# Optimization experiments

Hardware: AMD Instinct MI355X
Metric: run time of the kernel (lower is better)

The kernel has to match this reference:

```python
import jax, jax.numpy as jnp
import numpy as np
import math

DIM = 1024
NUM_HEAD = 16
HEAD_DIM = DIM // NUM_HEAD


def setup_inputs() -> dict:
    key = jax.random.key(0)
    ks = jax.random.split(key, 4)
    B, L = 4, 2048
    x = jax.random.normal(ks[0], (B, L, DIM), dtype=jnp.float32)
    # Linear weights stored as [in, out]; scaled like torch default init (~1/sqrt(in)).
    w_qkv = jax.random.normal(ks[1], (DIM, 3 * DIM), dtype=jnp.float32) / math.sqrt(DIM)
    b_qkv = jnp.zeros((3 * DIM,), dtype=jnp.float32)
    w_out = jax.random.normal(ks[2], (DIM, DIM), dtype=jnp.float32) / math.sqrt(DIM)
    b_out = jnp.zeros((DIM,), dtype=jnp.float32)
    return {"x": x, "w_qkv": w_qkv, "b_qkv": b_qkv, "w_out": w_out, "b_out": b_out}


def _attn(x, w_qkv, b_qkv, w_out, b_out):
    B, L, D = x.shape
    qkv = x @ w_qkv + b_qkv                      # [B, L, 3D]
    q, k, v = jnp.split(qkv, 3, axis=-1)         # each [B, L, D]
    def heads(t):
        return t.reshape(B, L, NUM_HEAD, HEAD_DIM).transpose(0, 2, 1, 3)  # [B,H,L,d]
    q, k, v = heads(q), heads(k), heads(v)
    scale = 1.0 / math.sqrt(HEAD_DIM)
    w = jnp.einsum('bhqd,bhkd->bhqk', q, k) * scale   # [B,H,L,L]
    causal = jnp.tril(jnp.ones((L, L), dtype=bool))
    w = jnp.where(causal, w, -jnp.inf)
    w = jax.nn.softmax(w, axis=-1)               # dropout_p = 0 -> identity
    out = jnp.einsum('bhqk,bhkd->bhqd', w, v)    # [B,H,L,d]
    out = out.transpose(0, 2, 1, 3).reshape(B, L, D)
    return out @ w_out + b_out


def reference(x, w_qkv, b_qkv, w_out, b_out):
    return _attn(x, w_qkv, b_qkv, w_out, b_out)
```

## Files before the change

### kernel.cpp

```cpp
#include <hip/hip_runtime.h>

typedef __bf16 bf16;
typedef __attribute__((ext_vector_type(8))) __bf16 bf16x8;
typedef __attribute__((ext_vector_type(4))) __bf16 bf16x4;
typedef __attribute__((ext_vector_type(4))) float f32x4;

#define MFMA16(a, b, c) __builtin_amdgcn_mfma_f32_16x16x32_bf16((a), (b), (c), 0, 0, 0)


static __device__ __forceinline__ bf16x8 cvt_f4x2(const float4 a, const float4 b) {
  bf16x8 r;
  r[0] = (bf16)a.x; r[1] = (bf16)a.y; r[2] = (bf16)a.z; r[3] = (bf16)a.w;
  r[4] = (bf16)b.x; r[5] = (bf16)b.y; r[6] = (bf16)b.z; r[7] = (bf16)b.w;
  return r;
}

static __device__ __forceinline__ void gll16(const bf16* g, bf16* l) {
  __builtin_amdgcn_global_load_lds(
      (const __attribute__((address_space(1))) void*)g,
      (__attribute__((address_space(3))) void*)l, 16, 0, 0);
}

__global__ __launch_bounds__(256) void conv_x_kernel(const float* __restrict__ X,
                                                     bf16* __restrict__ Xb) {
  const size_t i = ((size_t)blockIdx.x * 256 + threadIdx.x) * 16;
  const float4* s = (const float4*)&X[i];
  *(bf16x8*)&Xb[i] = cvt_f4x2(s[0], s[1]);
  *(bf16x8*)&Xb[i + 8] = cvt_f4x2(s[2], s[3]);
}

__global__ __launch_bounds__(256) void conv_w_kernel(
    const float* __restrict__ W, bf16* __restrict__ Wt, int Nw) {
  __shared__ bf16 sT[64][72];
  const int tid = threadIdx.x;
  const int n0 = blockIdx.x * 64, k0 = blockIdx.y * 64;
  const int kr = tid >> 4;
  const int c4 = (tid & 15) * 4;
#pragma unroll
  for (int i = 0; i < 4; ++i) {
    const int k = kr + i * 16;
    const float4 w4 = *(const float4*)&W[(size_t)(k0 + k) * Nw + n0 + c4];
    sT[c4 + 0][k] = (bf16)w4.x;
    sT[c4 + 1][k] = (bf16)w4.y;
    sT[c4 + 2][k] = (bf16)w4.z;
    sT[c4 + 3][k] = (bf16)w4.w;
  }
  __syncthreads();
  const int r = tid >> 2;
  const int c8 = (tid & 3) * 16;
  *(bf16x8*)&Wt[(size_t)(n0 + r) * 1024 + k0 + c8] = *(const bf16x8*)&sT[r][c8];
  *(bf16x8*)&Wt[(size_t)(n0 + r) * 1024 + k0 + c8 + 8] =
      *(const bf16x8*)&sT[r][c8 + 8];
}

static __device__ __forceinline__ void qkv_epilogue(
    f32x4 acc[4][4], const float* bias, bf16* Qb, bf16* Kb, bf16* Vt, int m0,
    int n0, int wr, int wc, int lg, int lr) {
  if (n0 < 2048) {
    bf16* dst = (n0 < 1024) ? Qb : Kb;
#pragma unroll
    for (int m = 0; m < 4; ++m) {
#pragma unroll
      for (int n = 0; n < 4; ++n) {
        const int colg = n0 + wc * 64 + n * 16 + lr;
        const int col = colg & 1023;
        const int h = col >> 6, d = col & 63;
        const float bv = bias[colg];
#pragma unroll
        for (int i = 0; i < 4; ++i) {
          const int row = m0 + wr * 64 + m * 16 + lg * 4 + i;
          const int bb = row >> 11, ll = row & 2047;
          dst[((size_t)((bb * 16 + h) * 2048 + ll)) * 64 + d] =
              (bf16)(acc[m][n][i] + bv);
        }
      }
    }
  } else {
#pragma unroll
    for (int m = 0; m < 4; ++m) {
#pragma unroll
      for (int n = 0; n < 4; ++n) {
        const int colg = n0 + wc * 64 + n * 16 + lr;
        const int col = colg & 1023;
        const int h = col >> 6, d = col & 63;
        const float bv = bias[colg];
        const int row0 = m0 + wr * 64 + m * 16 + lg * 4;
        const int bb = row0 >> 11, ll0 = row0 & 2047;
        bf16x4 pk;
#pragma unroll
        for (int i = 0; i < 4; ++i) pk[i] = (bf16)(acc[m][n][i] + bv);
        *(bf16x4*)&Vt[((size_t)((bb * 16 + h) * 64 + d)) * 2048 + ll0] = pk;
      }
    }
  }
}

__global__ __launch_bounds__(256) void gemm_qkv_bf16_kernel(
    const bf16* __restrict__ Xb, const bf16* __restrict__ Wt,
    const float* __restrict__ bias, bf16* __restrict__ Qb,
    bf16* __restrict__ Kb, bf16* __restrict__ Vt) {
  constexpr int K = 1024;
  __shared__ __align__(16) bf16 sA[128 * 64];
  __shared__ __align__(16) bf16 sB[128 * 64];
  const int tid = threadIdx.x;
  const int m0 = blockIdx.y * 128, n0 = blockIdx.x * 128;
  const int wid = tid >> 6, lane = tid & 63;
  const int wr = wid >> 1, wc = wid & 1;
  const int lg = lane >> 4, lr = lane & 15;

  const f32x4 fz = {0.f, 0.f, 0.f, 0.f};
  f32x4 acc[4][4];
#pragma unroll
  for (int m = 0; m < 4; ++m)
#pragma unroll
    for (int n = 0; n < 4; ++n) acc[m][n] = fz;

  for (int k0 = 0; k0 < K; k0 += 64) {
#pragma unroll
    for (int s = 0; s < 4; ++s) {
      const int off = s * 2048 + tid * 8;
      const int row = off >> 6, col = off & 63;
      gll16(&Xb[(size_t)(m0 + row) * K + k0 + col], &sA[off]);
      gll16(&Wt[(size_t)(n0 + row) * K + k0 + col], &sB[off]);
    }
    __syncthreads();

    bf16x8 af[2][4], bfv[2][4];
#pragma unroll
    for (int ks = 0; ks < 2; ++ks) {
#pragma unroll
      for (int m = 0; m < 4; ++m)
        af[ks][m] = *(const bf16x8*)&sA[(wr * 64 + m * 16 + lr) * 64 + ks * 32 + 8 * lg];
#pragma unroll
      for (int n = 0; n < 4; ++n)
        bfv[ks][n] = *(const bf16x8*)&sB[(wc * 64 + n * 16 + lr) * 64 + ks * 32 + 8 * lg];
    }
#pragma unroll
    for (int ks = 0; ks < 2; ++ks)
#pragma unroll
      for (int m = 0; m < 4; ++m)
#pragma unroll
        for (int n = 0; n < 4; ++n)
          acc[m][n] = MFMA16(af[ks][m], bfv[ks][n], acc[m][n]);
    __syncthreads();
  }
  qkv_epilogue(acc, bias, Qb, Kb, Vt, m0, n0, wr, wc, lg, lr);
}

__global__ __launch_bounds__(256) void gemm_qkv_kernel(
    const float* __restrict__ X, const bf16* __restrict__ Wt,
    const float* __restrict__ bias, bf16* __restrict__ Qb,
    bf16* __restrict__ Kb, bf16* __restrict__ Vt) {
  constexpr int K = 1024;
  __shared__ __align__(16) bf16 sA[128 * 64];
  __shared__ __align__(16) bf16 sB[128 * 64];
  const int tid = threadIdx.x;
  const int m0 = blockIdx.y * 128, n0 = blockIdx.x * 128;
  const int wid = tid >> 6, lane = tid & 63;
  const int wr = wid >> 1, wc = wid & 1;
  const int lg = lane >> 4, lr = lane & 15;

  const f32x4 fz = {0.f, 0.f, 0.f, 0.f};
  f32x4 acc[4][4];
#pragma unroll
  for (int m = 0; m < 4; ++m)
#pragma unroll
    for (int n = 0; n < 4; ++n) acc[m][n] = fz;

  for (int k0 = 0; k0 < K; k0 += 64) {
#pragma unroll
    for (int s = 0; s < 4; ++s) {
      const int off = s * 2048 + tid * 8;
      const int row = off >> 6, col = off & 63;
      gll16(&Wt[(size_t)(n0 + row) * K + k0 + col], &sB[off]);
    }
#pragma unroll
    for (int p = 0; p < 4; ++p) {
      const int g = tid + p * 256;
      const int row = g >> 3, c8 = (g & 7) * 8;
      const float4* src = (const float4*)&X[(size_t)(m0 + row) * K + k0 + c8];
      const float4 u = src[0], w = src[1];
      *(bf16x8*)&sA[row * 64 + c8] = cvt_f4x2(u, w);
    }
    __syncthreads();

    bf16x8 af[2][4], bfv[2][4];
#pragma unroll
    for (int ks = 0; ks < 2; ++ks) {
#pragma unroll
      for (int m = 0; m < 4; ++m)
        af[ks][m] = *(const bf16x8*)&sA[(wr * 64 + m * 16 + lr) * 64 + ks * 32 + 8 * lg];
#pragma unroll
      for (int n = 0; n < 4; ++n)
        bfv[ks][n] = *(const bf16x8*)&sB[(wc * 64 + n * 16 + lr) * 64 + ks * 32 + 8 * lg];
    }
#pragma unroll
    for (int ks = 0; ks < 2; ++ks)
#pragma unroll
      for (int m = 0; m < 4; ++m)
#pragma unroll
        for (int n = 0; n < 4; ++n)
          acc[m][n] = MFMA16(af[ks][m], bfv[ks][n], acc[m][n]);
    __syncthreads();
  }
  qkv_epilogue(acc, bias, Qb, Kb, Vt, m0, n0, wr, wc, lg, lr);
}

#define ATTN_FULL 0
#define ATTN_MASK 1
#define ATTN_SKIP 2

__global__ __launch_bounds__(256, 3) void attn_kernel(
    const bf16* __restrict__ Qb, const bf16* __restrict__ Kb,
    const bf16* __restrict__ Vt, bf16* __restrict__ O) {
  __shared__ __align__(16) bf16 sK[2][64 * 64];
  __shared__ __align__(16) bf16 sV[2][64 * 64];
  __shared__ __align__(16) bf16 sP[4][16 * 72];
  const int tid = threadIdx.x;
  const int qb = 15 - (int)(blockIdx.x >> 6);
  const int bh = blockIdx.x & 63;
  const int q0 = qb * 128;
  const int nt = 2 * qb + 2;
  const int wid = tid >> 6, lane = tid & 63;
  const int lg = lane >> 4, lr = lane & 15;
  const bf16* Kbh = Kb + (size_t)bh * (2048 * 64);
  const bf16* Vth = Vt + (size_t)bh * (64 * 2048);
  bf16* sPw = &sP[wid][0];
  const int swz = (lr & 7) << 3;

  const int qrow0 = q0 + wid * 16 + lr;
  const int qrow1 = qrow0 + 64;
  bf16x8 qf[2][2];
#pragma unroll
  for (int h = 0; h < 2; ++h) {
    const bf16* qp =
        Qb + (size_t)bh * (2048 * 64) + (size_t)(qrow0 + 64 * h) * 64 + 8 * lg;
    qf[h][0] = *(const bf16x8*)qp;
    qf[h][1] = *(const bf16x8*)(qp + 32);
#pragma unroll
    for (int j = 0; j < 8; ++j) {
      qf[h][0][j] = (bf16)((float)qf[h][0][j] * 0.125f);
      qf[h][1][j] = (bf16)((float)qf[h][1][j] * 0.125f);
    }
  }

  const int pe = tid * 8;
  const int srow0 = pe >> 6;
  const int scol0 = (pe & 63) ^ ((srow0 & 7) << 3);
  const int srow1 = srow0 + 32;
  const int scol1 = (pe & 63) ^ ((srow1 & 7) << 3);

  const f32x4 fz = {0.f, 0.f, 0.f, 0.f};
  f32x4 o[2][4];
#pragma unroll
  for (int h = 0; h < 2; ++h)
#pragma unroll
    for (int n = 0; n < 4; ++n) o[h][n] = fz;
  float m_[2] = {-1e30f, -1e30f}, ssum[2] = {0.f, 0.f};

#define STAGE(buf, kv0_)                                                      \
  {                                                                           \
    const int kv0s = (kv0_);                                                  \
    gll16(&Kbh[(size_t)(kv0s + srow0) * 64 + scol0], &sK[buf][pe]);           \
    gll16(&Kbh[(size_t)(kv0s + srow1) * 64 + scol1], &sK[buf][2048 + pe]);    \
    gll16(&Vth[(size_t)srow0 * 2048 + kv0s + scol0], &sV[buf][pe]);           \
    gll16(&Vth[(size_t)srow1 * 2048 + kv0s + scol1], &sV[buf][2048 + pe]);    \
  }

  STAGE(0, 0);

  for (int t = 0; t < nt; ++t) {
    const int buf = t & 1;
    const int kv0 = t * 64;
    const int mode0 = (t < nt - 2) ? ATTN_FULL : (t == nt - 2 ? ATTN_MASK : ATTN_SKIP);
    const int mode1 = (t < nt - 1) ? ATTN_FULL : ATTN_MASK;

    __builtin_amdgcn_s_barrier();
    if (t + 1 < nt) {
      STAGE(buf ^ 1, kv0 + 64);
      asm volatile("s_waitcnt vmcnt(4)" ::: "memory");
    } else {
      asm volatile("s_waitcnt vmcnt(0)" ::: "memory");
    }
    __builtin_amdgcn_s_barrier();

    const bf16* sKb = sK[buf];
    const bf16* sVb = sV[buf];

    f32x4 s0[4], s1[4];
    __builtin_amdgcn_s_setprio(1);
#pragma unroll
    for (int sub = 0; sub < 4; ++sub) {
      const int e = ((sub * 16 + lr) * 64 + 8 * lg) ^ swz;
      const bf16x8 kf0 = *(const bf16x8*)&sKb[e];
      const bf16x8 kf1 = *(const bf16x8*)&sKb[e ^ 32];
      if (mode0 != ATTN_SKIP) {
        f32x4 sc = MFMA16(kf0, qf[0][0], fz);
        s0[sub] = MFMA16(kf1, qf[0][1], sc);
      }
      f32x4 sc = MFMA16(kf0, qf[1][0], fz);
      s1[sub] = MFMA16(kf1, qf[1][1], sc);
    }
    __builtin_amdgcn_s_setprio(0);

    bf16x8 vf[4][2];
#pragma unroll
    for (int n = 0; n < 4; ++n)
#pragma unroll
      for (int c2 = 0; c2 < 2; ++c2)
        vf[n][c2] = *(const bf16x8*)&sVb[(((n * 16 + lr) * 64 + c2 * 32 + 8 * lg)) ^ swz];

#pragma unroll
    for (int h = 0; h < 2; ++h) {
      const int mode = h ? mode1 : mode0;
      if (mode == ATTN_SKIP) continue;
      const int qrow = h ? qrow1 : qrow0;
      f32x4* sh = h ? s1 : s0;

      float sv[16];
      float rm = -3e30f;
#pragma unroll
      for (int sub = 0; sub < 4; ++sub)
#pragma unroll
        for (int i = 0; i < 4; ++i) {
          float v = sh[sub][i];
          if (mode == ATTN_MASK) {
            const int kvg = kv0 + sub * 16 + lg * 4 + i;
            v = (kvg > qrow) ? -3e30f : v;
          }
          sv[sub * 4 + i] = v;
          rm = fmaxf(rm, v);
        }
      rm = fmaxf(rm, __shfl_xor(rm, 16));
      rm = fmaxf(rm, __shfl_xor(rm, 32));
      if (!__all(rm <= m_[h] + 8.f)) {
        const float mn = fmaxf(m_[h], rm);
        const float corr = __expf(m_[h] - mn);
        ssum[h] *= corr;
        m_[h] = mn;
        float cr[4];
#pragma unroll
        for (int i = 0; i < 4; ++i) cr[i] = __shfl(corr, 4 * lg + i);
#pragma unroll
        for (int n = 0; n < 4; ++n)
#pragma unroll
          for (int i = 0; i < 4; ++i) o[h][n][i] *= cr[i];
      }
      float rs = 0.f;
#pragma unroll
      for (int sub = 0; sub < 4; ++sub) {
        bf16x4 pk;
#pragma unroll
        for (int i = 0; i < 4; ++i) {
          const float p = __expf(sv[sub * 4 + i] - m_[h]);
          rs += p;
          pk[i] = (bf16)p;
        }
        *(bf16x4*)&sPw[lr * 72 + 16 * sub + 4 * lg] = pk;
      }
      rs += __shfl_xor(rs, 16);
      rs += __shfl_xor(rs, 32);
      ssum[h] += rs;
      __builtin_amdgcn_s_setprio(1);
#pragma unroll
      for (int c2 = 0; c2 < 2; ++c2) {
        const bf16x8 pf = *(const bf16x8*)&sPw[lr * 72 + 32 * c2 + 8 * lg];
#pragma unroll
        for (int n = 0; n < 4; ++n) o[h][n] = MFMA16(pf, vf[n][c2], o[h][n]);
      }
      __builtin_amdgcn_s_setprio(0);
    }
  }
#undef STAGE

  const int b = bh >> 4, hh = bh & 15;
#pragma unroll
  for (int h = 0; h < 2; ++h) {
    const float rinv = 1.f / ssum[h];
    float rv[4];
#pragma unroll
    for (int i = 0; i < 4; ++i) rv[i] = __shfl(rinv, 4 * lg + i);
#pragma unroll
    for (int n = 0; n < 4; ++n)
#pragma unroll
      for (int i = 0; i < 4; ++i) {
        const int q = q0 + 64 * h + wid * 16 + 4 * lg + i;
        O[((size_t)(b * 2048 + q)) * 1024 + hh * 64 + n * 16 + lr] =
            (bf16)(o[h][n][i] * rv[i]);
      }
  }
}

__global__ __launch_bounds__(256) void gemm_out_kernel(
    const bf16* __restrict__ A, const bf16* __restrict__ Wt,
    const float* __restrict__ bias, float* __restrict__ Out) {
  constexpr int K = 1024, N = 1024;
  __shared__ __align__(16) bf16 sA[128 * 64];
  __shared__ __align__(16) bf16 sB[128 * 64];
  const int tid = threadIdx.x;
  const int m0 = blockIdx.y * 128, n0 = blockIdx.x * 128;
  const int wid = tid >> 6, lane = tid & 63;
  const int wr = wid >> 1, wc = wid & 1;
  const int lg = lane >> 4, lr = lane & 15;

  const f32x4 fz = {0.f, 0.f, 0.f, 0.f};
  f32x4 acc[4][4];
#pragma unroll
  for (int m = 0; m < 4; ++m)
#pragma unroll
    for (int n = 0; n < 4; ++n) acc[m][n] = fz;

  for (int k0 = 0; k0 < K; k0 += 64) {
#pragma unroll
    for (int s = 0; s < 4; ++s) {
      const int off = s * 2048 + tid * 8;
      const int row = off >> 6, col = off & 63;
      gll16(&A[(size_t)(m0 + row) * K + k0 + col], &sA[off]);
      gll16(&Wt[(size_t)(n0 + row) * K + k0 + col], &sB[off]);
    }
    __syncthreads();

    bf16x8 af[2][4], bfv[2][4];
#pragma unroll
    for (int ks = 0; ks < 2; ++ks) {
#pragma unroll
      for (int m = 0; m < 4; ++m)
        af[ks][m] = *(const bf16x8*)&sA[(wr * 64 + m * 16 + lr) * 64 + ks * 32 + 8 * lg];
#pragma unroll
      for (int n = 0; n < 4; ++n)
        bfv[ks][n] = *(const bf16x8*)&sB[(wc * 64 + n * 16 + lr) * 64 + ks * 32 + 8 * lg];
    }
#pragma unroll
    for (int ks = 0; ks < 2; ++ks)
#pragma unroll
      for (int m = 0; m < 4; ++m)
#pragma unroll
        for (int n = 0; n < 4; ++n)
          acc[m][n] = MFMA16(af[ks][m], bfv[ks][n], acc[m][n]);
    __syncthreads();
  }

#pragma unroll
  for (int m = 0; m < 4; ++m) {
#pragma unroll
    for (int n = 0; n < 4; ++n) {
      const int colg = n0 + wc * 64 + n * 16 + lr;
      const float bv = bias[colg];
#pragma unroll
      for (int i = 0; i < 4; ++i) {
        const int row = m0 + wr * 64 + m * 16 + lg * 4 + i;
        Out[(size_t)row * N + colg] = acc[m][n][i] + bv;
      }
    }
  }
}

extern "C" void kernel_launch(void* const* d_in, const int* in_sizes, int n_in,
                              void* d_out, int out_size, void* d_ws,
                              size_t ws_size, hipStream_t stream) {
  const float* x     = (const float*)d_in[0];
  const float* w_qkv = (const float*)d_in[1];
  const float* b_qkv = (const float*)d_in[2];
  const float* w_out = (const float*)d_in[3];
  const float* b_out = (const float*)d_in[4];
  float* out = (float*)d_out;

  char* ws = (char*)d_ws;
  const size_t MB = 1024 * 1024;

  if (ws_size >= 70 * MB) {
    bf16* Xb  = (bf16*)(ws);
    bf16* Wt1 = (bf16*)(ws + 16 * MB);
    bf16* Qb  = (bf16*)(ws + 22 * MB);
    bf16* Kb  = (bf16*)(ws + 38 * MB);
    bf16* Vt  = (bf16*)(ws + 54 * MB);
    bf16* Ab  = (bf16*)(ws);
    bf16* Wt2 = (bf16*)(ws + 16 * MB);

    conv_x_kernel<<<dim3(2048), 256, 0, stream>>>(x, Xb);
    conv_w_kernel<<<dim3(48, 16), 256, 0, stream>>>(w_qkv, Wt1, 3072);
    gemm_qkv_bf16_kernel<<<dim3(24, 64), 256, 0, stream>>>(Xb, Wt1, b_qkv, Qb, Kb, Vt);
    attn_kernel<<<dim3(1024), 256, 0, stream>>>(Qb, Kb, Vt, Ab);
    conv_w_kernel<<<dim3(16, 16), 256, 0, stream>>>(w_out, Wt2, 1024);
    gemm_out_kernel<<<dim3(8, 64), 256, 0, stream>>>(Ab, Wt2, b_out, out);
  } else {
    bf16* Qb  = (bf16*)(ws);
    bf16* Kb  = (bf16*)(ws + 16 * MB);
    bf16* Vt  = (bf16*)(ws + 32 * MB);
    bf16* Wt1 = (bf16*)(ws + 48 * MB);
    bf16* Ab  = (bf16*)(ws + 48 * MB);
    bf16* Wt2 = (bf16*)(ws);

    conv_w_kernel<<<dim3(48, 16), 256, 0, stream>>>(w_qkv, Wt1, 3072);
    gemm_qkv_kernel<<<dim3(24, 64), 256, 0, stream>>>(x, Wt1, b_qkv, Qb, Kb, Vt);
    attn_kernel<<<dim3(1024), 256, 0, stream>>>(Qb, Kb, Vt, Ab);
    conv_w_kernel<<<dim3(16, 16), 256, 0, stream>>>(w_out, Wt2, 1024);
    gemm_out_kernel<<<dim3(8, 64), 256, 0, stream>>>(Ab, Wt2, b_out, out);
  }
}
```

Before: 326.9 us.

## Double-buffer GEMM loads, swizzle tiles, fuse conversions, use exp2 in softmax

The QKV and output GEMMs get double-buffered LDS tiles: the next k-slice is prefetched through global_load_lds while the current one is multiplied, and a 1D grid with a grouped tile swizzle is meant to improve L2 reuse. The x and w_qkv fp32-to-bf16 conversions are merged into one launch. The w_out conversion is moved ahead of attention. In attention, the log2(e) factor is folded into the Q scale so softmax can use hardware exp2, with the rescale threshold adjusted to match. Doubling LDS per block may reduce occupancy, and the hand-written vmcnt waits depend on the exact count of outstanding loads.

```diff
diff --git a/kernel.cpp b/kernel.cpp
--- a/kernel.cpp
+++ b/kernel.cpp
@@ -6,6 +6,12 @@
 typedef __attribute__((ext_vector_type(4))) float f32x4;
 
 #define MFMA16(a, b, c) __builtin_amdgcn_mfma_f32_16x16x32_bf16((a), (b), (c), 0, 0, 0)
+
+#if __has_builtin(__builtin_amdgcn_exp2f)
+#define EXP2(x) __builtin_amdgcn_exp2f(x)
+#else
+#define EXP2(x) exp2f(x)
+#endif
 
 
 static __device__ __forceinline__ bf16x8 cvt_f4x2(const float4 a, const float4 b) {
@@ -21,12 +27,38 @@
       (__attribute__((address_space(3))) void*)l, 16, 0, 0);
 }
 
-__global__ __launch_bounds__(256) void conv_x_kernel(const float* __restrict__ X,
-                                                     bf16* __restrict__ Xb) {
-  const size_t i = ((size_t)blockIdx.x * 256 + threadIdx.x) * 16;
-  const float4* s = (const float4*)&X[i];
-  *(bf16x8*)&Xb[i] = cvt_f4x2(s[0], s[1]);
-  *(bf16x8*)&Xb[i + 8] = cvt_f4x2(s[2], s[3]);
+__global__ __launch_bounds__(256) void conv_all_kernel(
+    const float* __restrict__ X, bf16* __restrict__ Xb,
+    const float* __restrict__ W1, bf16* __restrict__ Wt1) {
+  __shared__ bf16 sT[64][72];
+  const int bid = blockIdx.x;
+  const int tid = threadIdx.x;
+  if (bid < 2048) {
+    const size_t i = ((size_t)bid * 256 + tid) * 16;
+    const float4* s = (const float4*)&X[i];
+    *(bf16x8*)&Xb[i] = cvt_f4x2(s[0], s[1]);
+    *(bf16x8*)&Xb[i + 8] = cvt_f4x2(s[2], s[3]);
+    return;
+  }
+  const int cb = bid - 2048;
+  const int n0 = (cb % 48) * 64, k0 = (cb / 48) * 64;
+  const int kr = tid >> 4;
+  const int c4 = (tid & 15) * 4;
+#pragma unroll
+  for (int i = 0; i < 4; ++i) {
+    const int k = kr + i * 16;
+    const float4 w4 = *(const float4*)&W1[(size_t)(k0 + k) * 3072 + n0 + c4];
+    sT[c4 + 0][k] = (bf16)w4.x;
+    sT[c4 + 1][k] = (bf16)w4.y;
+    sT[c4 + 2][k] = (bf16)w4.z;
+    sT[c4 + 3][k] = (bf16)w4.w;
+  }
+  __syncthreads();
+  const int r = tid >> 2;
+  const int c8 = (tid & 3) * 16;
+  *(bf16x8*)&Wt1[(size_t)(n0 + r) * 1024 + k0 + c8] = *(const bf16x8*)&sT[r][c8];
+  *(bf16x8*)&Wt1[(size_t)(n0 + r) * 1024 + k0 + c8 + 8] =
+      *(const bf16x8*)&sT[r][c8 + 8];
 }
 
 __global__ __launch_bounds__(256) void conv_w_kernel(
@@ -95,15 +127,17 @@
   }
 }
 
-__global__ __launch_bounds__(256) void gemm_qkv_bf16_kernel(
+__global__ __launch_bounds__(256, 2) void gemm_qkv_bf16_kernel(
     const bf16* __restrict__ Xb, const bf16* __restrict__ Wt,
     const float* __restrict__ bias, bf16* __restrict__ Qb,
     bf16* __restrict__ Kb, bf16* __restrict__ Vt) {
-  constexpr int K = 1024;
-  __shared__ __align__(16) bf16 sA[128 * 64];
-  __shared__ __align__(16) bf16 sB[128 * 64];
+  constexpr int K = 1024, NT = K / 64;
+  __shared__ __align__(16) bf16 sA[2][128 * 64];
+  __shared__ __align__(16) bf16 sB[2][128 * 64];
   const int tid = threadIdx.x;
-  const int m0 = blockIdx.y * 128, n0 = blockIdx.x * 128;
+  const int id = blockIdx.x;
+  const int swz = (id & 7) * 192 + (id >> 3);
+  const int m0 = (swz & 63) * 128, n0 = (swz >> 6) * 128;
   const int wid = tid >> 6, lane = tid & 63;
   const int wr = wid >> 1, wc = wid & 1;
   const int lg = lane >> 4, lr = lane & 15;
@@ -115,35 +149,46 @@
 #pragma unroll
     for (int n = 0; n < 4; ++n) acc[m][n] = fz;
 
-  for (int k0 = 0; k0 < K; k0 += 64) {
-#pragma unroll
-    for (int s = 0; s < 4; ++s) {
-      const int off = s * 2048 + tid * 8;
-      const int row = off >> 6, col = off & 63;
-      gll16(&Xb[(size_t)(m0 + row) * K + k0 + col], &sA[off]);
-      gll16(&Wt[(size_t)(n0 + row) * K + k0 + col], &sB[off]);
-    }
-    __syncthreads();
-
-    bf16x8 af[2][4], bfv[2][4];
+#define GSTAGE(buf, k0_)                                                \
+  {                                                                     \
+    const int k0s = (k0_);                                              \
+    _Pragma("unroll") for (int s = 0; s < 4; ++s) {                     \
+      const int o = s * 2048 + tid * 8;                                 \
+      const int row = o >> 6, col = o & 63;                             \
+      gll16(&Xb[(size_t)(m0 + row) * K + k0s + col], &sA[buf][o]);      \
+      gll16(&Wt[(size_t)(n0 + row) * K + k0s + col], &sB[buf][o]);      \
+    }                                                                   \
+  }
+
+  GSTAGE(0, 0);
+  for (int t = 0; t < NT; ++t) {
+    const int buf = t & 1;
+    __builtin_amdgcn_s_barrier();
+    if (t + 1 < NT) {
+      GSTAGE(buf ^ 1, (t + 1) * 64);
+      asm volatile("s_waitcnt vmcnt(8)" ::: "memory");
+    } else {
+      asm volatile("s_waitcnt vmcnt(0)" ::: "memory");
+    }
+    __builtin_amdgcn_s_barrier();
+
 #pragma unroll
     for (int ks = 0; ks < 2; ++ks) {
+      bf16x8 af[4], bfv[4];
 #pragma unroll
       for (int m = 0; m < 4; ++m)
-        af[ks][m] = *(const bf16x8*)&sA[(wr * 64 + m * 16 + lr) * 64 + ks * 32 + 8 * lg];
+        af[m] = *(const bf16x8*)&sA[buf][(wr * 64 + m * 16 + lr) * 64 + ks * 32 + 8 * lg];
 #pragma unroll
       for (int n = 0; n < 4; ++n)
-        bfv[ks][n] = *(const bf16x8*)&sB[(wc * 64 + n * 16 + lr) * 64 + ks * 32 + 8 * lg];
-    }
-#pragma unroll
-    for (int ks = 0; ks < 2; ++ks)
+        bfv[n] = *(const bf16x8*)&sB[buf][(wc * 64 + n * 16 + lr) * 64 + ks * 32 + 8 * lg];
 #pragma unroll
       for (int m = 0; m < 4; ++m)
 #pragma unroll
         for (int n = 0; n < 4; ++n)
-          acc[m][n] = MFMA16(af[ks][m], bfv[ks][n], acc[m][n]);
-    __syncthreads();
-  }
+          acc[m][n] = MFMA16(af[m], bfv[n], acc[m][n]);
+    }
+  }
+#undef GSTAGE
   qkv_epilogue(acc, bias, Qb, Kb, Vt, m0, n0, wr, wc, lg, lr);
 }
 
@@ -184,23 +229,21 @@
     }
     __syncthreads();
 
-    bf16x8 af[2][4], bfv[2][4];
 #pragma unroll
     for (int ks = 0; ks < 2; ++ks) {
+      bf16x8 af[4], bfv[4];
 #pragma unroll
       for (int m = 0; m < 4; ++m)
-        af[ks][m] = *(const bf16x8*)&sA[(wr * 64 + m * 16 + lr) * 64 + ks * 32 + 8 * lg];
+        af[m] = *(const bf16x8*)&sA[(wr * 64 + m * 16 + lr) * 64 + ks * 32 + 8 * lg];
 #pragma unroll
       for (int n = 0; n < 4; ++n)
-        bfv[ks][n] = *(const bf16x8*)&sB[(wc * 64 + n * 16 + lr) * 64 + ks * 32 + 8 * lg];
-    }
-#pragma unroll
-    for (int ks = 0; ks < 2; ++ks)
+        bfv[n] = *(const bf16x8*)&sB[(wc * 64 + n * 16 + lr) * 64 + ks * 32 + 8 * lg];
 #pragma unroll
       for (int m = 0; m < 4; ++m)
 #pragma unroll
         for (int n = 0; n < 4; ++n)
-          acc[m][n] = MFMA16(af[ks][m], bfv[ks][n], acc[m][n]);
+          acc[m][n] = MFMA16(af[m], bfv[n], acc[m][n]);
+    }
     __syncthreads();
   }
   qkv_epilogue(acc, bias, Qb, Kb, Vt, m0, n0, wr, wc, lg, lr);
@@ -228,6 +271,7 @@
   bf16* sPw = &sP[wid][0];
   const int swz = (lr & 7) << 3;
 
+  const float qsc = 0.125f * 1.44269504089f;
   const int qrow0 = q0 + wid * 16 + lr;
   const int qrow1 = qrow0 + 64;
   bf16x8 qf[2][2];
@@ -239,8 +283,8 @@
     qf[h][1] = *(const bf16x8*)(qp + 32);
 #pragma unroll
     for (int j = 0; j < 8; ++j) {
-      qf[h][0][j] = (bf16)((float)qf[h][0][j] * 0.125f);
-      qf[h][1][j] = (bf16)((float)qf[h][1][j] * 0.125f);
+      qf[h][0][j] = (bf16)((float)qf[h][0][j] * qsc);
+      qf[h][1][j] = (bf16)((float)qf[h][1][j] * qsc);
     }
   }
 
@@ -333,9 +377,9 @@
         }
       rm = fmaxf(rm, __shfl_xor(rm, 16));
       rm = fmaxf(rm, __shfl_xor(rm, 32));
-      if (!__all(rm <= m_[h] + 8.f)) {
+      if (!__all(rm <= m_[h] + 11.54f)) {
         const float mn = fmaxf(m_[h], rm);
-        const float corr = __expf(m_[h] - mn);
+        const float corr = EXP2(m_[h] - mn);
         ssum[h] *= corr;
         m_[h] = mn;
         float cr[4];
@@ -352,7 +396,7 @@
         bf16x4 pk;
 #pragma unroll
         for (int i = 0; i < 4; ++i) {
-          const float p = __expf(sv[sub * 4 + i] - m_[h]);
+          const float p = EXP2(sv[sub * 4 + i] - m_[h]);
           rs += p;
           pk[i] = (bf16)p;
         }
@@ -391,14 +435,16 @@
   }
 }
 
-__global__ __launch_bounds__(256) void gemm_out_kernel(
+__global__ __launch_bounds__(256, 2) void gemm_out_kernel(
     const bf16* __restrict__ A, const bf16* __restrict__ Wt,
     const float* __restrict__ bias, float* __restrict__ Out) {
-  constexpr int K = 1024, N = 1024;
-  __shared__ __align__(16) bf16 sA[128 * 64];
-  __shared__ __align__(16) bf16 sB[128 * 64];
+  constexpr int K = 1024, N = 1024, NT = K / 64;
+  __shared__ __align__(16) bf16 sA[2][128 * 64];
+  __shared__ __align__(16) bf16 sB[2][128 * 64];
   const int tid = threadIdx.x;
-  const int m0 = blockIdx.y * 128, n0 = blockIdx.x * 128;
+  const int id = blockIdx.x;
+  const int swz = (id & 7) * 64 + (id >> 3);
+  const int m0 = (swz & 63) * 128, n0 = (swz >> 6) * 128;
   const int wid = tid >> 6, lane = tid & 63;
   const int wr = wid >> 1, wc = wid & 1;
   const int lg = lane >> 4, lr = lane & 15;
@@ -410,35 +456,46 @@
 #pragma unroll
     for (int n = 0; n < 4; ++n) acc[m][n] = fz;
 
-  for (int k0 = 0; k0 < K; k0 += 64) {
-#pragma unroll
-    for (int s = 0; s < 4; ++s) {
-      const int off = s * 2048 + tid * 8;
-      const int row = off >> 6, col = off & 63;
-      gll16(&A[(size_t)(m0 + row) * K + k0 + col], &sA[off]);
-      gll16(&Wt[(size_t)(n0 + row) * K + k0 + col], &sB[off]);
-    }
-    __syncthreads();
-
-    bf16x8 af[2][4], bfv[2][4];
+#define GSTAGE(buf, k0_)                                               \
+  {                                                                    \
+    const int k0s = (k0_);                                             \
+    _Pragma("unroll") for (int s = 0; s < 4; ++s) {                    \
+      const int o = s * 2048 + tid * 8;                                \
+      const int row = o >> 6, col = o & 63;                            \
+      gll16(&A[(size_t)(m0 + row) * K + k0s + col], &sA[buf][o]);      \
+      gll16(&Wt[(size_t)(n0 + row) * K + k0s + col], &sB[buf][o]);     \
+    }                                                                  \
+  }
+
+  GSTAGE(0, 0);
+  for (int t = 0; t < NT; ++t) {
+    const int buf = t & 1;
+    __builtin_amdgcn_s_barrier();
+    if (t + 1 < NT) {
+      GSTAGE(buf ^ 1, (t + 1) * 64);
+      asm volatile("s_waitcnt vmcnt(8)" ::: "memory");
+    } else {
+      asm volatile("s_waitcnt vmcnt(0)" ::: "memory");
+    }
+    __builtin_amdgcn_s_barrier();
+
 #pragma unroll
     for (int ks = 0; ks < 2; ++ks) {
+      bf16x8 af[4], bfv[4];
 #pragma unroll
       for (int m = 0; m < 4; ++m)
-        af[ks][m] = *(const bf16x8*)&sA[(wr * 64 + m * 16 + lr) * 64 + ks * 32 + 8 * lg];
+        af[m] = *(const bf16x8*)&sA[buf][(wr * 64 + m * 16 + lr) * 64 + ks * 32 + 8 * lg];
 #pragma unroll
       for (int n = 0; n < 4; ++n)
-        bfv[ks][n] = *(const bf16x8*)&sB[(wc * 64 + n * 16 + lr) * 64 + ks * 32 + 8 * lg];
-    }
-#pragma unroll
-    for (int ks = 0; ks < 2; ++ks)
+        bfv[n] = *(const bf16x8*)&sB[buf][(wc * 64 + n * 16 + lr) * 64 + ks * 32 + 8 * lg];
 #pragma unroll
       for (int m = 0; m < 4; ++m)
 #pragma unroll
         for (int n = 0; n < 4; ++n)
-          acc[m][n] = MFMA16(af[ks][m], bfv[ks][n], acc[m][n]);
-    __syncthreads();
-  }
+          acc[m][n] = MFMA16(af[m], bfv[n], acc[m][n]);
+    }
+  }
+#undef GSTAGE
 
 #pragma unroll
   for (int m = 0; m < 4; ++m) {
@@ -477,12 +534,11 @@
     bf16* Ab  = (bf16*)(ws);
     bf16* Wt2 = (bf16*)(ws + 16 * MB);
 
-    conv_x_kernel<<<dim3(2048), 256, 0, stream>>>(x, Xb);
-    conv_w_kernel<<<dim3(48, 16), 256, 0, stream>>>(w_qkv, Wt1, 3072);
-    gemm_qkv_bf16_kernel<<<dim3(24, 64), 256, 0, stream>>>(Xb, Wt1, b_qkv, Qb, Kb, Vt);
+    conv_all_kernel<<<dim3(2816), 256, 0, stream>>>(x, Xb, w_qkv, Wt1);
+    gemm_qkv_bf16_kernel<<<dim3(1536), 256, 0, stream>>>(Xb, Wt1, b_qkv, Qb, Kb, Vt);
+    conv_w_kernel<<<dim3(16, 16), 256, 0, stream>>>(w_out, Wt2, 1024);
     attn_kernel<<<dim3(1024), 256, 0, stream>>>(Qb, Kb, Vt, Ab);
-    conv_w_kernel<<<dim3(16, 16), 256, 0, stream>>>(w_out, Wt2, 1024);
-    gemm_out_kernel<<<dim3(8, 64), 256, 0, stream>>>(Ab, Wt2, b_out, out);
+    gemm_out_kernel<<<dim3(512), 256, 0, stream>>>(Ab, Wt2, b_out, out);
   } else {
     bf16* Qb  = (bf16*)(ws);
     bf16* Kb  = (bf16*)(ws + 16 * MB);
@@ -495,6 +551,6 @@
     gemm_qkv_kernel<<<dim3(24, 64), 256, 0, stream>>>(x, Wt1, b_qkv, Qb, Kb, Vt);
     attn_kernel<<<dim3(1024), 256, 0, stream>>>(Qb, Kb, Vt, Ab);
     conv_w_kernel<<<dim3(16, 16), 256, 0, stream>>>(w_out, Wt2, 1024);
-    gemm_out_kernel<<<dim3(8, 64), 256, 0, stream>>>(Ab, Wt2, b_out, out);
-  }
-}
+    gemm_out_kernel<<<dim3(512), 256, 0, stream>>>(Ab, Wt2, b_out, out);
+  }
+}
```

After: 326.8 us. About the same (-0.0%).
